# Kernel tuning notes

Hardware: AMD Instinct MI355X
Metric: run time of the kernel (lower is better)

## Reference

```python
import jax, jax.numpy as jnp
import numpy as np

NUM_USERS = 100000
NUM_ITEMS = 100000
EMB_DIM = 64
NUM_NODES = NUM_USERS + NUM_ITEMS
NUM_EDGES = 4000000
BATCH = 4096
NUM_LAYERS = 2


def setup_inputs() -> dict:
    key = jax.random.key(0)
    ks = jax.random.split(key, 8)
    user = jax.random.randint(ks[0], (BATCH,), 0, NUM_USERS, dtype=jnp.int64) if jax.config.jax_enable_x64 else jax.random.randint(ks[0], (BATCH,), 0, NUM_USERS, dtype=jnp.int32)
    pos = jax.random.randint(ks[1], (BATCH,), 0, NUM_ITEMS, dtype=jnp.int32)
    neg = jax.random.randint(ks[2], (BATCH,), 0, NUM_ITEMS, dtype=jnp.int32)
    edge_row = jax.random.randint(ks[3], (NUM_EDGES,), 0, NUM_NODES, dtype=jnp.int32)
    edge_col = jax.random.randint(ks[4], (NUM_EDGES,), 0, NUM_NODES, dtype=jnp.int32)
    # normalized adjacency values (degree-normalized in real LightGCN)
    edge_val = jax.random.uniform(ks[5], (NUM_EDGES,), dtype=jnp.float32) * 0.01
    user_emb = jax.random.normal(ks[6], (NUM_USERS, EMB_DIM), dtype=jnp.float32) * 0.01
    item_emb = jax.random.normal(ks[7], (NUM_ITEMS, EMB_DIM), dtype=jnp.float32) * 0.01
    return {"user": user, "pos": pos, "neg": neg,
            "edge_row": edge_row, "edge_col": edge_col, "edge_val": edge_val,
            "user_emb": user_emb, "item_emb": item_emb}


def _spmm(edge_row, edge_col, edge_val, x):
    # out[r] = sum_e val[e] * x[col[e]]  -- sparse adjacency times dense emb
    msgs = edge_val[:, None] * x[edge_col]  # [E, D]
    return jax.ops.segment_sum(msgs, edge_row, num_segments=NUM_NODES)


def reference(user, pos, neg, edge_row, edge_col, edge_val, user_emb, item_emb):
    all_emb = jnp.concatenate([user_emb, item_emb], axis=0)  # [N, D]
    acc = all_emb
    h = all_emb
    for _ in range(NUM_LAYERS):
        h = _spmm(edge_row, edge_col, edge_val, h)
        acc = acc + h
    lightgcn_out = acc / (NUM_LAYERS + 1)  # mean over stacked layer embeddings
    u = lightgcn_out[:NUM_USERS]
    i = lightgcn_out[NUM_USERS:]
    user_latent = u[user]          # [B, D]
    positive_latent = i[pos]       # [B, D]
    negative_latent = i[neg]       # [B, D]
    positive_score = jnp.sum(user_latent * positive_latent, axis=1)
    negative_score = jnp.sum(user_latent * negative_latent, axis=1)
    return positive_score, negative_score
```

## Files before the change

kernel.cpp:

```cpp
#include <hip/hip_runtime.h>
#include <cstdint>
#include <cstddef>

#define NUM_USERS 100000
#define NUM_ITEMS 100000
#define NUM_NODES 200000
#define NUM_EDGES 4000000
#define BATCH     4096
#define EMB       64

#define NB    782
#define CAP   5632
#define CHUNK 16384
#define PTHREADS 1024
#define EPB   16


__device__ __forceinline__ unsigned short f2bf(float f) {
    unsigned u = __float_as_uint(f);
    u = (u + 0x7FFFu + ((u >> 16) & 1u)) >> 16;
    return (unsigned short)u;
}
__device__ __forceinline__ float bf2f(unsigned short b) {
    return __uint_as_float(((unsigned)b) << 16);
}


__global__ void k_cvt(const float* __restrict__ uemb, const float* __restrict__ iemb,
                      unsigned short* __restrict__ xb) {
    int i = blockIdx.x * blockDim.x + threadIdx.x;
    const int TOT8 = (NUM_NODES * EMB) / 8;
    if (i >= TOT8) return;
    size_t off = (size_t)i * 8;
    const size_t UELEMS = (size_t)NUM_USERS * EMB;
    const float* src = (off < UELEMS) ? (uemb + off) : (iemb + (off - UELEMS));
    float4 f0 = ((const float4*)src)[0];
    float4 f1 = ((const float4*)src)[1];
    ushort4 o0 = make_ushort4(f2bf(f0.x), f2bf(f0.y), f2bf(f0.z), f2bf(f0.w));
    ushort4 o1 = make_ushort4(f2bf(f1.x), f2bf(f1.y), f2bf(f1.z), f2bf(f1.w));
    ((ushort4*)(xb + off))[0] = o0;
    ((ushort4*)(xb + off))[1] = o1;
}


__global__ void k_binit(int* __restrict__ bcur) {
    int b = blockIdx.x * blockDim.x + threadIdx.x;
    if (b < NB) bcur[b] = b * CAP;
}

__global__ void k_part1(const int* __restrict__ erow, const int* __restrict__ ecol,
                        const float* __restrict__ eval_, int* __restrict__ bcur,
                        int2* __restrict__ tmp) {
    __shared__ int hist[NB];
    __shared__ int base[NB];
    int t = threadIdx.x;
    int start = blockIdx.x * CHUNK;
    for (int i = t; i < NB; i += PTHREADS) hist[i] = 0;
    __syncthreads();
    int rows[EPB], ranks[EPB];
#pragma unroll
    for (int k = 0; k < EPB; ++k) {
        int e = start + t + k * PTHREADS;
        if (e < NUM_EDGES) {
            int r = erow[e];
            rows[k]  = r;
            ranks[k] = atomicAdd(&hist[r >> 8], 1);
        } else {
            rows[k] = -1;
        }
    }
    __syncthreads();
    for (int i = t; i < NB; i += PTHREADS) {
        int c = hist[i];
        base[i] = c ? atomicAdd(&bcur[i], c) : 0;
    }
    __syncthreads();
#pragma unroll
    for (int k = 0; k < EPB; ++k) {
        int e = start + t + k * PTHREADS;
        if (rows[k] >= 0) {
            int r   = rows[k];
            int bkt = r >> 8;
            int pos = base[bkt] + ranks[k];
            if (pos < (bkt + 1) * CAP)
                tmp[pos] = make_int2(((r & 255) << 24) | ecol[e], __float_as_int(eval_[e]));
        }
    }
}

__global__ void k_bscan(const int* __restrict__ bcur, int* __restrict__ bbase) {
    __shared__ int lds[1024];
    int t = threadIdx.x;
    int v = 0;
    if (t < NB) v = min(bcur[t] - t * CAP, CAP);
    lds[t] = v;
    __syncthreads();
    for (int off = 1; off < 1024; off <<= 1) {
        int add = (t >= off) ? lds[t - off] : 0;
        __syncthreads();
        lds[t] += add;
        __syncthreads();
    }
    int ex = lds[t] - v;
    if (t < NB) bbase[t] = ex;
    if (t == NB - 1) bbase[NB] = lds[t];
}

__global__ void k_part2(const int* __restrict__ bbase, const int2* __restrict__ tmp,
                        int2* __restrict__ epack, int* __restrict__ row_ptr) {
    __shared__ int cnt[256];
    __shared__ int sc[256];
    __shared__ int loc[256];
    int b = blockIdx.x, t = threadIdx.x;
    int base_row = b << 8;
    int nrows = min(256, NUM_NODES - base_row);
    int s0 = b * CAP;
    int nb_cnt = bbase[b + 1] - bbase[b];
    int obase = bbase[b];
    if (t < 256) cnt[t] = 0;
    __syncthreads();
    for (int i = t; i < nb_cnt; i += 512)
        atomicAdd(&cnt[((unsigned)tmp[s0 + i].x) >> 24], 1);
    __syncthreads();
    int v = 0;
    if (t < 256) { v = cnt[t]; sc[t] = v; }
    __syncthreads();
    for (int off = 1; off < 256; off <<= 1) {
        int add = 0;
        if (t < 256 && t >= off) add = sc[t - off];
        __syncthreads();
        if (t < 256 && t >= off) sc[t] += add;
        __syncthreads();
    }
    if (t < 256) {
        int cur = obase + sc[t] - v;
        if (t < nrows) row_ptr[base_row + t] = cur;
        loc[t] = cur;
    }
    __syncthreads();
    for (int i = t; i < nb_cnt; i += 512) {
        int2 rec = tmp[s0 + i];
        int pos = atomicAdd(&loc[((unsigned)rec.x) >> 24], 1);
        epack[pos] = make_int2(rec.x & 0xFFFFFF, rec.y);
    }
    if (b == 0 && t == 0) row_ptr[NUM_NODES] = NUM_EDGES;
}


__global__ void k_spmm1(const int* __restrict__ row_ptr, const int2* __restrict__ epack,
                        const unsigned short* __restrict__ xb,
                        unsigned short* __restrict__ h1) {
    int wid  = (blockIdx.x * blockDim.x + threadIdx.x) >> 6;
    int lane = threadIdx.x & 63;
    if (wid >= NUM_NODES) return;
    int g = lane >> 4;
    int q = (lane & 15) * 4;
    int s = row_ptr[wid];
    int t = row_ptr[wid + 1];
    float a0 = 0.f, a1 = 0.f, a2 = 0.f, a3 = 0.f;
    for (int e = s; e < t; e += 8) {
        int eA = e + g, eB = e + 4 + g;
        int2 pA = epack[eA < t ? eA : s];
        int2 pB = epack[eB < t ? eB : s];
        float vA = (eA < t) ? __int_as_float(pA.y) : 0.f;
        float vB = (eB < t) ? __int_as_float(pB.y) : 0.f;
        ushort4 xA = *(const ushort4*)(xb + (size_t)pA.x * EMB + q);
        ushort4 xB = *(const ushort4*)(xb + (size_t)pB.x * EMB + q);
        a0 = fmaf(vA, bf2f(xA.x), a0); a1 = fmaf(vA, bf2f(xA.y), a1);
        a2 = fmaf(vA, bf2f(xA.z), a2); a3 = fmaf(vA, bf2f(xA.w), a3);
        a0 = fmaf(vB, bf2f(xB.x), a0); a1 = fmaf(vB, bf2f(xB.y), a1);
        a2 = fmaf(vB, bf2f(xB.z), a2); a3 = fmaf(vB, bf2f(xB.w), a3);
    }
    a0 += __shfl_xor(a0, 16, 64); a1 += __shfl_xor(a1, 16, 64);
    a2 += __shfl_xor(a2, 16, 64); a3 += __shfl_xor(a3, 16, 64);
    a0 += __shfl_xor(a0, 32, 64); a1 += __shfl_xor(a1, 32, 64);
    a2 += __shfl_xor(a2, 32, 64); a3 += __shfl_xor(a3, 32, 64);
    if (lane < 16) {
        ushort4 o = make_ushort4(f2bf(a0), f2bf(a1), f2bf(a2), f2bf(a3));
        *(ushort4*)(h1 + (size_t)wid * EMB + q) = o;
    }
}


__device__ __forceinline__ const float* node_ptr(int c, const float* __restrict__ uemb,
                                                 const float* __restrict__ iemb) {
    return (c < NUM_USERS) ? (uemb + (size_t)c * EMB)
                           : (iemb + (size_t)(c - NUM_USERS) * EMB);
}

__global__ void k_final(const int* __restrict__ user, const int* __restrict__ pos,
                        const int* __restrict__ neg,
                        const int* __restrict__ row_ptr, const int2* __restrict__ epack,
                        const float* __restrict__ uemb, const float* __restrict__ iemb,
                        const unsigned short* __restrict__ h1, float* __restrict__ out) {
    __shared__ float lds[3 * EMB];
    int b    = blockIdx.x;
    int w    = threadIdx.x >> 6;
    int lane = threadIdx.x & 63;
    int g = lane >> 4;
    int q = (lane & 15) * 4;

    int node;
    if (w == 0)      node = user[b];
    else if (w == 1) node = NUM_USERS + pos[b];
    else             node = NUM_USERS + neg[b];

    int s = row_ptr[node];
    int t = row_ptr[node + 1];
    float a0 = 0.f, a1 = 0.f, a2 = 0.f, a3 = 0.f;
    for (int e = s; e < t; e += 8) {
        int eA = e + g, eB = e + 4 + g;
        int2 pA = epack[eA < t ? eA : s];
        int2 pB = epack[eB < t ? eB : s];
        float vA = (eA < t) ? __int_as_float(pA.y) : 0.f;
        float vB = (eB < t) ? __int_as_float(pB.y) : 0.f;
        ushort4 yA = *(const ushort4*)(h1 + (size_t)pA.x * EMB + q);
        ushort4 yB = *(const ushort4*)(h1 + (size_t)pB.x * EMB + q);
        a0 = fmaf(vA, bf2f(yA.x), a0); a1 = fmaf(vA, bf2f(yA.y), a1);
        a2 = fmaf(vA, bf2f(yA.z), a2); a3 = fmaf(vA, bf2f(yA.w), a3);
        a0 = fmaf(vB, bf2f(yB.x), a0); a1 = fmaf(vB, bf2f(yB.y), a1);
        a2 = fmaf(vB, bf2f(yB.z), a2); a3 = fmaf(vB, bf2f(yB.w), a3);
    }
    a0 += __shfl_xor(a0, 16, 64); a1 += __shfl_xor(a1, 16, 64);
    a2 += __shfl_xor(a2, 16, 64); a3 += __shfl_xor(a3, 16, 64);
    a0 += __shfl_xor(a0, 32, 64); a1 += __shfl_xor(a1, 32, 64);
    a2 += __shfl_xor(a2, 32, 64); a3 += __shfl_xor(a3, 32, 64);

    if (lane < 16) {
        const float* xbp = node_ptr(node, uemb, iemb) + q;
        float4  xd = *(const float4*)xbp;
        ushort4 hn = *(const ushort4*)(h1 + (size_t)node * EMB + q);
        a0 = (a0 + xd.x + bf2f(hn.x)) / 3.0f;
        a1 = (a1 + xd.y + bf2f(hn.y)) / 3.0f;
        a2 = (a2 + xd.z + bf2f(hn.z)) / 3.0f;
        a3 = (a3 + xd.w + bf2f(hn.w)) / 3.0f;
        *(float4*)(lds + w * EMB + q) = make_float4(a0, a1, a2, a3);
    }
    __syncthreads();

    if (w < 2) {
        float prod = lds[lane] * lds[(w + 1) * EMB + lane];
        for (int off = 32; off; off >>= 1) prod += __shfl_xor(prod, off, 64);
        if (lane == 0) out[w * BATCH + b] = prod;
    }
}


extern "C" void kernel_launch(void* const* d_in, const int* in_sizes, int n_in,
                              void* d_out, int out_size, void* d_ws, size_t ws_size,
                              hipStream_t stream) {
    const int*   user  = (const int*)d_in[0];
    const int*   pos   = (const int*)d_in[1];
    const int*   neg   = (const int*)d_in[2];
    const int*   erow  = (const int*)d_in[3];
    const int*   ecol  = (const int*)d_in[4];
    const float* eval_ = (const float*)d_in[5];
    const float* uemb  = (const float*)d_in[6];
    const float* iemb  = (const float*)d_in[7];
    float* out = (float*)d_out;

    char* ws = (char*)d_ws;
    unsigned short* xb = (unsigned short*)(ws);
    unsigned short* h1 = (unsigned short*)(ws + 25600000);
    int2* tmp     = (int2*)(ws + 25600000);
    int*  row_ptr = (int*)(ws + 60833792);
    int*  bbase   = (int*)(ws + 61633856);
    int*  bcur    = (int*)(ws + 61637952);
    int2* epack   = (int2*)(ws + 61642048);

    k_cvt<<<((NUM_NODES * EMB) / 8 + 255) / 256, 256, 0, stream>>>(uemb, iemb, xb);
    k_binit<<<(NB + 255) / 256, 256, 0, stream>>>(bcur);

    k_part1<<<(NUM_EDGES + CHUNK - 1) / CHUNK, PTHREADS, 0, stream>>>(erow, ecol, eval_,
                                                                      bcur, tmp);
    k_bscan<<<1, 1024, 0, stream>>>(bcur, bbase);
    k_part2<<<NB, 512, 0, stream>>>(bbase, tmp, epack, row_ptr);

    k_spmm1<<<(NUM_NODES * 64 + 255) / 256, 256, 0, stream>>>(row_ptr, epack, xb, h1);

    k_final<<<BATCH, 192, 0, stream>>>(user, pos, neg, row_ptr, epack,
                                       uemb, iemb, h1, out);
}
```

Measured before the change: 361.2 us.

## Fuse bucket sort with first-layer SpMM in LDS and compact batch-node edges

Merges the per-bucket row sort (part2) with the first SpMM layer: each block sorts its bucket's edges into shared memory and immediately computes h1 for its 256 rows, removing the bucket scan kernel, the global CSR write and the epack reread. Edges of rows that appear in the batch are copied into a compact side buffer so the final layer reads only those, avoiding a full row_ptr. Buffer initialisation and batch marking are folded into the convert kernel. The fused kernel holds a large shared-memory array (CAP int2, about 45 KB), which may reduce occupancy, and it adds a memset plus a global atomic.

```diff
diff --git a/kernel.cpp b/kernel.cpp
--- a/kernel.cpp
+++ b/kernel.cpp
@@ -14,6 +14,7 @@
 #define CHUNK 16384
 #define PTHREADS 1024
 #define EPB   16
+#define SIDE_CAP 1048576
 
 
 __device__ __forceinline__ unsigned short f2bf(float f) {
@@ -27,8 +28,18 @@
 
 
 __global__ void k_cvt(const float* __restrict__ uemb, const float* __restrict__ iemb,
-                      unsigned short* __restrict__ xb) {
+                      unsigned short* __restrict__ xb, int* __restrict__ bcur,
+                      int* __restrict__ gcur,
+                      const int* __restrict__ user, const int* __restrict__ pos,
+                      const int* __restrict__ neg, unsigned char* __restrict__ mark) {
     int i = blockIdx.x * blockDim.x + threadIdx.x;
+    if (i < NB) bcur[i] = i * CAP;
+    if (i == 0) *gcur = 0;
+    if (i < BATCH) {
+        mark[user[i]] = 1;
+        mark[NUM_USERS + pos[i]] = 1;
+        mark[NUM_USERS + neg[i]] = 1;
+    }
     const int TOT8 = (NUM_NODES * EMB) / 8;
     if (i >= TOT8) return;
     size_t off = (size_t)i * 8;
@@ -43,11 +54,6 @@
 }
 
 
-__global__ void k_binit(int* __restrict__ bcur) {
-    int b = blockIdx.x * blockDim.x + threadIdx.x;
-    if (b < NB) bcur[b] = b * CAP;
-}
-
 __global__ void k_part1(const int* __restrict__ erow, const int* __restrict__ ecol,
                         const float* __restrict__ eval_, int* __restrict__ bcur,
                         int2* __restrict__ tmp) {
@@ -88,26 +94,14 @@
     }
 }
 
-__global__ void k_bscan(const int* __restrict__ bcur, int* __restrict__ bbase) {
-    __shared__ int lds[1024];
-    int t = threadIdx.x;
-    int v = 0;
-    if (t < NB) v = min(bcur[t] - t * CAP, CAP);
-    lds[t] = v;
-    __syncthreads();
-    for (int off = 1; off < 1024; off <<= 1) {
-        int add = (t >= off) ? lds[t - off] : 0;
-        __syncthreads();
-        lds[t] += add;
-        __syncthreads();
-    }
-    int ex = lds[t] - v;
-    if (t < NB) bbase[t] = ex;
-    if (t == NB - 1) bbase[NB] = lds[t];
-}
-
-__global__ void k_part2(const int* __restrict__ bbase, const int2* __restrict__ tmp,
-                        int2* __restrict__ epack, int* __restrict__ row_ptr) {
+
+__global__ void k_bspmm(const int* __restrict__ bcur, const int2* __restrict__ tmp,
+                        const unsigned short* __restrict__ xb,
+                        unsigned short* __restrict__ h1,
+                        const unsigned char* __restrict__ mark,
+                        int2* __restrict__ row_se, int2* __restrict__ side,
+                        int* __restrict__ gcur) {
+    __shared__ int2 srec[CAP];
     __shared__ int cnt[256];
     __shared__ int sc[256];
     __shared__ int loc[256];
@@ -115,11 +109,11 @@
     int base_row = b << 8;
     int nrows = min(256, NUM_NODES - base_row);
     int s0 = b * CAP;
-    int nb_cnt = bbase[b + 1] - bbase[b];
-    int obase = bbase[b];
+    int n = min(bcur[b] - s0, CAP);
+
     if (t < 256) cnt[t] = 0;
     __syncthreads();
-    for (int i = t; i < nb_cnt; i += 512)
+    for (int i = t; i < n; i += 512)
         atomicAdd(&cnt[((unsigned)tmp[s0 + i].x) >> 24], 1);
     __syncthreads();
     int v = 0;
@@ -132,52 +126,54 @@
         if (t < 256 && t >= off) sc[t] += add;
         __syncthreads();
     }
-    if (t < 256) {
-        int cur = obase + sc[t] - v;
-        if (t < nrows) row_ptr[base_row + t] = cur;
-        loc[t] = cur;
-    }
-    __syncthreads();
-    for (int i = t; i < nb_cnt; i += 512) {
+    if (t < 256) loc[t] = sc[t] - v;
+    __syncthreads();
+    for (int i = t; i < n; i += 512) {
         int2 rec = tmp[s0 + i];
         int pos = atomicAdd(&loc[((unsigned)rec.x) >> 24], 1);
-        epack[pos] = make_int2(rec.x & 0xFFFFFF, rec.y);
-    }
-    if (b == 0 && t == 0) row_ptr[NUM_NODES] = NUM_EDGES;
-}
-
-
-__global__ void k_spmm1(const int* __restrict__ row_ptr, const int2* __restrict__ epack,
-                        const unsigned short* __restrict__ xb,
-                        unsigned short* __restrict__ h1) {
-    int wid  = (blockIdx.x * blockDim.x + threadIdx.x) >> 6;
-    int lane = threadIdx.x & 63;
-    if (wid >= NUM_NODES) return;
-    int g = lane >> 4;
-    int q = (lane & 15) * 4;
-    int s = row_ptr[wid];
-    int t = row_ptr[wid + 1];
-    float a0 = 0.f, a1 = 0.f, a2 = 0.f, a3 = 0.f;
-    for (int e = s; e < t; e += 8) {
-        int eA = e + g, eB = e + 4 + g;
-        int2 pA = epack[eA < t ? eA : s];
-        int2 pB = epack[eB < t ? eB : s];
-        float vA = (eA < t) ? __int_as_float(pA.y) : 0.f;
-        float vB = (eB < t) ? __int_as_float(pB.y) : 0.f;
-        ushort4 xA = *(const ushort4*)(xb + (size_t)pA.x * EMB + q);
-        ushort4 xB = *(const ushort4*)(xb + (size_t)pB.x * EMB + q);
-        a0 = fmaf(vA, bf2f(xA.x), a0); a1 = fmaf(vA, bf2f(xA.y), a1);
-        a2 = fmaf(vA, bf2f(xA.z), a2); a3 = fmaf(vA, bf2f(xA.w), a3);
-        a0 = fmaf(vB, bf2f(xB.x), a0); a1 = fmaf(vB, bf2f(xB.y), a1);
-        a2 = fmaf(vB, bf2f(xB.z), a2); a3 = fmaf(vB, bf2f(xB.w), a3);
-    }
-    a0 += __shfl_xor(a0, 16, 64); a1 += __shfl_xor(a1, 16, 64);
-    a2 += __shfl_xor(a2, 16, 64); a3 += __shfl_xor(a3, 16, 64);
-    a0 += __shfl_xor(a0, 32, 64); a1 += __shfl_xor(a1, 32, 64);
-    a2 += __shfl_xor(a2, 32, 64); a3 += __shfl_xor(a3, 32, 64);
-    if (lane < 16) {
-        ushort4 o = make_ushort4(f2bf(a0), f2bf(a1), f2bf(a2), f2bf(a3));
-        *(ushort4*)(h1 + (size_t)wid * EMB + q) = o;
+        srec[pos] = rec;
+    }
+    __syncthreads();
+
+    int w = t >> 6, lane = t & 63;
+    int g = lane >> 4, q = (lane & 15) * 4;
+    for (int k = 0; k < 32; ++k) {
+        int r = w + (k << 3);
+        if (r >= nrows) break;
+        int end = loc[r], start = end - cnt[r];
+        float a0 = 0.f, a1 = 0.f, a2 = 0.f, a3 = 0.f;
+        for (int e = start; e < end; e += 8) {
+            int iA = e + g, iB = e + 4 + g;
+            int2 pA = srec[iA < end ? iA : start];
+            int2 pB = srec[iB < end ? iB : start];
+            float vA = (iA < end) ? __int_as_float(pA.y) : 0.f;
+            float vB = (iB < end) ? __int_as_float(pB.y) : 0.f;
+            int cA = pA.x & 0xFFFFFF, cB = pB.x & 0xFFFFFF;
+            ushort4 xA = *(const ushort4*)(xb + (size_t)cA * EMB + q);
+            ushort4 xB = *(const ushort4*)(xb + (size_t)cB * EMB + q);
+            a0 = fmaf(vA, bf2f(xA.x), a0); a1 = fmaf(vA, bf2f(xA.y), a1);
+            a2 = fmaf(vA, bf2f(xA.z), a2); a3 = fmaf(vA, bf2f(xA.w), a3);
+            a0 = fmaf(vB, bf2f(xB.x), a0); a1 = fmaf(vB, bf2f(xB.y), a1);
+            a2 = fmaf(vB, bf2f(xB.z), a2); a3 = fmaf(vB, bf2f(xB.w), a3);
+        }
+        a0 += __shfl_xor(a0, 16, 64); a1 += __shfl_xor(a1, 16, 64);
+        a2 += __shfl_xor(a2, 16, 64); a3 += __shfl_xor(a3, 16, 64);
+        a0 += __shfl_xor(a0, 32, 64); a1 += __shfl_xor(a1, 32, 64);
+        a2 += __shfl_xor(a2, 32, 64); a3 += __shfl_xor(a3, 32, 64);
+        if (lane < 16) {
+            ushort4 o = make_ushort4(f2bf(a0), f2bf(a1), f2bf(a2), f2bf(a3));
+            *(ushort4*)(h1 + (size_t)(base_row + r) * EMB + q) = o;
+        }
+        if (mark[base_row + r]) {
+            int rcnt = end - start;
+            int p = 0;
+            if (lane == 0) p = atomicAdd(gcur, rcnt);
+            p = __shfl(p, 0, 64);
+            if (lane == 0)
+                row_se[base_row + r] = make_int2(p, (p + rcnt <= SIDE_CAP) ? rcnt : 0);
+            if (p + rcnt <= SIDE_CAP)
+                for (int i2 = lane; i2 < rcnt; i2 += 64) side[p + i2] = srec[start + i2];
+        }
     }
 }
 
@@ -190,7 +186,7 @@
 
 __global__ void k_final(const int* __restrict__ user, const int* __restrict__ pos,
                         const int* __restrict__ neg,
-                        const int* __restrict__ row_ptr, const int2* __restrict__ epack,
+                        const int2* __restrict__ row_se, const int2* __restrict__ side,
                         const float* __restrict__ uemb, const float* __restrict__ iemb,
                         const unsigned short* __restrict__ h1, float* __restrict__ out) {
     __shared__ float lds[3 * EMB];
@@ -205,17 +201,18 @@
     else if (w == 1) node = NUM_USERS + pos[b];
     else             node = NUM_USERS + neg[b];
 
-    int s = row_ptr[node];
-    int t = row_ptr[node + 1];
+    int2 se = row_se[node];
+    int p = se.x, cn = se.y;
     float a0 = 0.f, a1 = 0.f, a2 = 0.f, a3 = 0.f;
-    for (int e = s; e < t; e += 8) {
-        int eA = e + g, eB = e + 4 + g;
-        int2 pA = epack[eA < t ? eA : s];
-        int2 pB = epack[eB < t ? eB : s];
-        float vA = (eA < t) ? __int_as_float(pA.y) : 0.f;
-        float vB = (eB < t) ? __int_as_float(pB.y) : 0.f;
-        ushort4 yA = *(const ushort4*)(h1 + (size_t)pA.x * EMB + q);
-        ushort4 yB = *(const ushort4*)(h1 + (size_t)pB.x * EMB + q);
+    for (int e = 0; e < cn; e += 8) {
+        int iA = e + g, iB = e + 4 + g;
+        int2 pA = side[p + (iA < cn ? iA : 0)];
+        int2 pB = side[p + (iB < cn ? iB : 0)];
+        float vA = (iA < cn) ? __int_as_float(pA.y) : 0.f;
+        float vB = (iB < cn) ? __int_as_float(pB.y) : 0.f;
+        int cA = pA.x & 0xFFFFFF, cB = pB.x & 0xFFFFFF;
+        ushort4 yA = *(const ushort4*)(h1 + (size_t)cA * EMB + q);
+        ushort4 yB = *(const ushort4*)(h1 + (size_t)cB * EMB + q);
         a0 = fmaf(vA, bf2f(yA.x), a0); a1 = fmaf(vA, bf2f(yA.y), a1);
         a2 = fmaf(vA, bf2f(yA.z), a2); a3 = fmaf(vA, bf2f(yA.w), a3);
         a0 = fmaf(vB, bf2f(yB.x), a0); a1 = fmaf(vB, bf2f(yB.y), a1);
@@ -262,22 +259,23 @@
     char* ws = (char*)d_ws;
     unsigned short* xb = (unsigned short*)(ws);
     unsigned short* h1 = (unsigned short*)(ws + 25600000);
-    int2* tmp     = (int2*)(ws + 25600000);
-    int*  row_ptr = (int*)(ws + 60833792);
-    int*  bbase   = (int*)(ws + 61633856);
-    int*  bcur    = (int*)(ws + 61637952);
-    int2* epack   = (int2*)(ws + 61642048);
-
-    k_cvt<<<((NUM_NODES * EMB) / 8 + 255) / 256, 256, 0, stream>>>(uemb, iemb, xb);
-    k_binit<<<(NB + 255) / 256, 256, 0, stream>>>(bcur);
+    int2* tmp     = (int2*)(ws + 51200000);
+    int2* row_se  = (int2*)(ws + 86433792);
+    int*  bcur    = (int*)(ws + 88033792);
+    int*  gcur    = (int*)(ws + 88037888);
+    unsigned char* mark = (unsigned char*)(ws + 88041984);
+    int2* side    = (int2*)(ws + 88242688);
+
+    hipMemsetAsync(mark, 0, NUM_NODES, stream);
+
+    k_cvt<<<((NUM_NODES * EMB) / 8 + 255) / 256, 256, 0, stream>>>(
+        uemb, iemb, xb, bcur, gcur, user, pos, neg, mark);
 
     k_part1<<<(NUM_EDGES + CHUNK - 1) / CHUNK, PTHREADS, 0, stream>>>(erow, ecol, eval_,
                                                                       bcur, tmp);
-    k_bscan<<<1, 1024, 0, stream>>>(bcur, bbase);
-    k_part2<<<NB, 512, 0, stream>>>(bbase, tmp, epack, row_ptr);
-
-    k_spmm1<<<(NUM_NODES * 64 + 255) / 256, 256, 0, stream>>>(row_ptr, epack, xb, h1);
-
-    k_final<<<BATCH, 192, 0, stream>>>(user, pos, neg, row_ptr, epack,
+
+    k_bspmm<<<NB, 512, 0, stream>>>(bcur, tmp, xb, h1, mark, row_se, side, gcur);
+
+    k_final<<<BATCH, 192, 0, stream>>>(user, pos, neg, row_se, side,
                                        uemb, iemb, h1, out);
 }
```

Measured after the change: 425.3 us. 1.18x slower.
